# Kernel tuning notes

Hardware: AMD Instinct MI355X
Metric: run time of the kernel (lower is better)

## Reference

```python
import jax, jax.numpy as jnp
import numpy as np

N = 4096      # 2 ** var_num, var_num = 12
L = 50        # trajectory length
A_NUM = 4     # number of action variables (len(id2actvar))


def setup_inputs() -> dict:
    key = jax.random.key(0)
    ks = jax.random.split(key, 6)
    scale = 0.5 / np.sqrt(N)  # keep recurrence spectrally stable over L steps
    return {
        "init_states": jax.random.normal(ks[0], (N,), dtype=jnp.float32),
        "trajectories": jax.random.uniform(ks[1], (L, A_NUM), dtype=jnp.float32),
        "T_base": jax.random.normal(ks[2], (N, N), dtype=jnp.float32) * scale,
        "A_mats": jax.random.normal(ks[3], (A_NUM, N, N), dtype=jnp.float32) * (scale / A_NUM),
        "b": jax.random.normal(ks[4], (N,), dtype=jnp.float32) * 0.1,
        "r": jax.random.normal(ks[5], (N,), dtype=jnp.float32),
    }


def reference(init_states, trajectories, T_base, A_mats, b, r):
    # init_states is read from x in the original model but never used in the loop.
    n = T_base.shape[0]
    interface0 = jnp.zeros((n,), dtype=T_base.dtype)  # tf.zeros(2**var_num)

    def step(old_interface, act):
        # action-conditioned circuit filter: T_t = T_base + sum_a act[a] * A_mats[a]
        T = T_base + jnp.einsum('a,anm->nm', act, A_mats)
        new_interface = T @ old_interface + b          # [N]
        exp_reward = jnp.sum(r * new_interface)        # tf.reduce_sum(exp_reward)
        return new_interface, exp_reward

    _, exp_rewards = jax.lax.scan(step, interface0, trajectories)
    return exp_rewards  # [L]
```

## Files before the change

### kernel.cpp

```cpp
#include <hip/hip_runtime.h>
#include <hip/hip_fp16.h>

#define NDIM  4096
#define LSTEPS 50
#define ANUM   4
#define NMATS  5

__global__ void init_kernel(const float* __restrict__ b, const float* __restrict__ r,
                            float* __restrict__ x1, float* __restrict__ out) {
    const int tid = threadIdx.x;
    if (tid < LSTEPS) out[tid] = 0.0f;
    float part = 0.0f;
    for (int i = tid; i < NDIM; i += 256) {
        float bi = b[i];
        x1[i] = bi;
        part += r[i] * bi;
    }
#pragma unroll
    for (int off = 32; off > 0; off >>= 1) part += __shfl_xor(part, off, 64);
    __shared__ float sm[4];
    const int wave = tid >> 6, lane = tid & 63;
    if (lane == 0) sm[wave] = part;
    __syncthreads();
    if (tid == 0) out[0] = sm[0] + sm[1] + sm[2] + sm[3];
}

__global__ void conv_kernel(const float* __restrict__ Tb, const float* __restrict__ Am,
                            uint4* __restrict__ dst) {
    const size_t idx  = (size_t)blockIdx.x * 256 + threadIdx.x;
    const size_t base = idx * 8;
    const size_t nn   = (size_t)NDIM * NDIM;
    const float4* src;
    size_t off4;
    if (base < nn) { src = (const float4*)Tb; off4 = base >> 2; }
    else           { src = (const float4*)Am; off4 = (base - nn) >> 2; }
    const float4 f0 = src[off4];
    const float4 f1 = src[off4 + 1];
    union { uint4 v; __half h[8]; } pk;
    pk.h[0] = __float2half(f0.x); pk.h[1] = __float2half(f0.y);
    pk.h[2] = __float2half(f0.z); pk.h[3] = __float2half(f0.w);
    pk.h[4] = __float2half(f1.x); pk.h[5] = __float2half(f1.y);
    pk.h[6] = __float2half(f1.z); pk.h[7] = __float2half(f1.w);
    dst[idx] = pk.v;
}

__global__ __launch_bounds__(256) void step_half(
        const uint4* __restrict__ mats,
        const float* __restrict__ x_in,
        float*       __restrict__ x_out,
        const float* __restrict__ b,
        const float* __restrict__ r,
        const float* __restrict__ traj,
        float*       __restrict__ out, int t) {
    __shared__ float xs[NDIM];
    __shared__ float parts[4];
    const int tid = threadIdx.x;
    {
        const float4* xv  = (const float4*)x_in;
        float4*       xsv = (float4*)xs;
#pragma unroll
        for (int i = 0; i < 4; i++) xsv[tid + 256 * i] = xv[tid + 256 * i];
    }
    __syncthreads();

    const float a0 = traj[t * ANUM + 0], a1 = traj[t * ANUM + 1],
                a2 = traj[t * ANUM + 2], a3 = traj[t * ANUM + 3];

    const int wave = tid >> 6, lane = tid & 63;
    const int row  = blockIdx.x * 4 + wave;
    const size_t matq = (size_t)NDIM * NDIM / 8;
    const size_t rowq = (size_t)row * (NDIM / 8);

    float acc[NMATS] = {0.f, 0.f, 0.f, 0.f, 0.f};
#pragma unroll
    for (int c = 0; c < 8; c++) {
        const float4* xp = (const float4*)(&xs[c * 512 + lane * 8]);
        const float4 xa = xp[0], xb = xp[1];
        const size_t qi = rowq + (size_t)c * 64 + lane;
#pragma unroll
        for (int m = 0; m < NMATS; m++) {
            union { uint4 v; __half2 h2[4]; } u;
            u.v = mats[(size_t)m * matq + qi];
            const float2 p0 = __half22float2(u.h2[0]);
            const float2 p1 = __half22float2(u.h2[1]);
            const float2 p2 = __half22float2(u.h2[2]);
            const float2 p3 = __half22float2(u.h2[3]);
            float a = acc[m];
            a = fmaf(p0.x, xa.x, a); a = fmaf(p0.y, xa.y, a);
            a = fmaf(p1.x, xa.z, a); a = fmaf(p1.y, xa.w, a);
            a = fmaf(p2.x, xb.x, a); a = fmaf(p2.y, xb.y, a);
            a = fmaf(p3.x, xb.z, a); a = fmaf(p3.y, xb.w, a);
            acc[m] = a;
        }
    }
    float s = acc[0] + a0 * acc[1] + a1 * acc[2] + a2 * acc[3] + a3 * acc[4];
#pragma unroll
    for (int off = 32; off > 0; off >>= 1) s += __shfl_xor(s, off, 64);
    if (lane == 0) {
        const float y = s + b[row];
        x_out[row] = y;
        parts[wave] = r[row] * y;
    }
    __syncthreads();
    if (tid == 0) atomicAdd(out + t, parts[0] + parts[1] + parts[2] + parts[3]);
}

__global__ __launch_bounds__(256) void step_f32(
        const float* __restrict__ Tb, const float* __restrict__ Am,
        const float* __restrict__ x_in, float* __restrict__ x_out,
        const float* __restrict__ b, const float* __restrict__ r,
        const float* __restrict__ traj, float* __restrict__ out, int t) {
    __shared__ float xs[NDIM];
    __shared__ float parts[4];
    const int tid = threadIdx.x;
    {
        const float4* xv  = (const float4*)x_in;
        float4*       xsv = (float4*)xs;
#pragma unroll
        for (int i = 0; i < 4; i++) xsv[tid + 256 * i] = xv[tid + 256 * i];
    }
    __syncthreads();

    const float a0 = traj[t * ANUM + 0], a1 = traj[t * ANUM + 1],
                a2 = traj[t * ANUM + 2], a3 = traj[t * ANUM + 3];

    const int wave = tid >> 6, lane = tid & 63;
    const int row  = blockIdx.x * 4 + wave;
    const size_t nn = (size_t)NDIM * NDIM;
    const float4* mat[NMATS] = {
        (const float4*)Tb, (const float4*)Am, (const float4*)(Am + nn),
        (const float4*)(Am + 2 * nn), (const float4*)(Am + 3 * nn)};
    const size_t rowq = (size_t)row * (NDIM / 4);

    float acc[NMATS] = {0.f, 0.f, 0.f, 0.f, 0.f};
#pragma unroll
    for (int c = 0; c < 16; c++) {
        const float4 xa = *(const float4*)(&xs[c * 256 + lane * 4]);
        const size_t qi = rowq + (size_t)c * 64 + lane;
#pragma unroll
        for (int m = 0; m < NMATS; m++) {
            const float4 v = mat[m][qi];
            float a = acc[m];
            a = fmaf(v.x, xa.x, a); a = fmaf(v.y, xa.y, a);
            a = fmaf(v.z, xa.z, a); a = fmaf(v.w, xa.w, a);
            acc[m] = a;
        }
    }
    float s = acc[0] + a0 * acc[1] + a1 * acc[2] + a2 * acc[3] + a3 * acc[4];
#pragma unroll
    for (int off = 32; off > 0; off >>= 1) s += __shfl_xor(s, off, 64);
    if (lane == 0) {
        const float y = s + b[row];
        x_out[row] = y;
        parts[wave] = r[row] * y;
    }
    __syncthreads();
    if (tid == 0) atomicAdd(out + t, parts[0] + parts[1] + parts[2] + parts[3]);
}

extern "C" void kernel_launch(void* const* d_in, const int* in_sizes, int n_in,
                              void* d_out, int out_size, void* d_ws, size_t ws_size,
                              hipStream_t stream) {
    const float* traj = (const float*)d_in[1];
    const float* Tb   = (const float*)d_in[2];
    const float* Am   = (const float*)d_in[3];
    const float* b    = (const float*)d_in[4];
    const float* r    = (const float*)d_in[5];
    float* out = (float*)d_out;

    const size_t matBytes = (size_t)NMATS * NDIM * NDIM * sizeof(__half);
    const size_t xBytes   = 2 * (size_t)NDIM * sizeof(float);
    const bool useHalf = ws_size >= matBytes + xBytes;

    if (useHalf) {
        uint4* mats = (uint4*)d_ws;
        float* x0 = (float*)((char*)d_ws + matBytes);
        float* x1 = x0 + NDIM;
        init_kernel<<<1, 256, 0, stream>>>(b, r, x0, out);
        const int convBlocks = (int)(((size_t)NMATS * NDIM * NDIM / 8) / 256);
        conv_kernel<<<convBlocks, 256, 0, stream>>>(Tb, Am, mats);
        for (int t = 1; t < LSTEPS; t++) {
            float* xi = (t & 1) ? x0 : x1;
            float* xo = (t & 1) ? x1 : x0;
            step_half<<<NDIM / 4, 256, 0, stream>>>(mats, xi, xo, b, r, traj, out, t);
        }
    } else {
        float* x0 = (float*)d_ws;
        float* x1 = x0 + NDIM;
        init_kernel<<<1, 256, 0, stream>>>(b, r, x0, out);
        for (int t = 1; t < LSTEPS; t++) {
            float* xi = (t & 1) ? x0 : x1;
            float* xo = (t & 1) ? x1 : x0;
            step_f32<<<NDIM / 4, 256, 0, stream>>>(Tb, Am, xi, xo, b, r, traj, out, t);
        }
    }
}
```

Before: 1.987 ms.

## Precombine per-step fp16 matrices in chunks so each step reads one matrix

Instead of converting five matrices to fp16 once and streaming all five every step, a combine kernel folds T_base plus the action-weighted A_mats into one fp16 matrix per timestep, in two chunks of 25 and 24 steps. Each step then streams one 32MB matrix instead of five. The per-step reward is no longer accumulated with atomics; an extra block computes the dot product of the previous state, which drops the zero-init dependency. The cost is a large combine write (about 800MB per chunk) and a much larger workspace requirement, and nontemporal loads are used for the matrix stream.

```diff
diff --git a/kernel.cpp b/kernel.cpp
--- a/kernel.cpp
+++ b/kernel.cpp
@@ -1,145 +1,180 @@
 #include <hip/hip_runtime.h>
 #include <hip/hip_fp16.h>
 
-#define NDIM  4096
+#define NDIM   4096
 #define LSTEPS 50
 #define ANUM   4
-#define NMATS  5
-
-__global__ void init_kernel(const float* __restrict__ b, const float* __restrict__ r,
-                            float* __restrict__ x1, float* __restrict__ out) {
+#define NN     ((size_t)NDIM * (size_t)NDIM)
+#define CHUNK1 25
+#define CHUNK2 24
+
+typedef unsigned int nuint4 __attribute__((ext_vector_type(4)));
+typedef float        nfloat4 __attribute__((ext_vector_type(4)));
+
+__global__ void init_kernel(const float* __restrict__ b, float* __restrict__ x1) {
     const int tid = threadIdx.x;
-    if (tid < LSTEPS) out[tid] = 0.0f;
-    float part = 0.0f;
-    for (int i = tid; i < NDIM; i += 256) {
-        float bi = b[i];
-        x1[i] = bi;
-        part += r[i] * bi;
-    }
-#pragma unroll
-    for (int off = 32; off > 0; off >>= 1) part += __shfl_xor(part, off, 64);
-    __shared__ float sm[4];
-    const int wave = tid >> 6, lane = tid & 63;
-    if (lane == 0) sm[wave] = part;
+    const float4* bv = (const float4*)b;
+    float4* xv = (float4*)x1;
+#pragma unroll
+    for (int i = 0; i < 4; i++) xv[tid + 256 * i] = bv[tid + 256 * i];
+}
+
+__global__ __launch_bounds__(256) void combine_kernel(
+        const float* __restrict__ Tb, const float* __restrict__ Am,
+        const float* __restrict__ traj, uint4* __restrict__ outbuf,
+        int t0, int C) {
+    __shared__ float sact[CHUNK1 * ANUM];
+    const int tid = threadIdx.x;
+    if (tid < C * ANUM)
+        sact[tid] = traj[(size_t)(t0 + tid / ANUM) * ANUM + (tid % ANUM)];
     __syncthreads();
-    if (tid == 0) out[0] = sm[0] + sm[1] + sm[2] + sm[3];
-}
-
-__global__ void conv_kernel(const float* __restrict__ Tb, const float* __restrict__ Am,
-                            uint4* __restrict__ dst) {
-    const size_t idx  = (size_t)blockIdx.x * 256 + threadIdx.x;
-    const size_t base = idx * 8;
-    const size_t nn   = (size_t)NDIM * NDIM;
-    const float4* src;
-    size_t off4;
-    if (base < nn) { src = (const float4*)Tb; off4 = base >> 2; }
-    else           { src = (const float4*)Am; off4 = (base - nn) >> 2; }
-    const float4 f0 = src[off4];
-    const float4 f1 = src[off4 + 1];
-    union { uint4 v; __half h[8]; } pk;
-    pk.h[0] = __float2half(f0.x); pk.h[1] = __float2half(f0.y);
-    pk.h[2] = __float2half(f0.z); pk.h[3] = __float2half(f0.w);
-    pk.h[4] = __float2half(f1.x); pk.h[5] = __float2half(f1.y);
-    pk.h[6] = __float2half(f1.z); pk.h[7] = __float2half(f1.w);
-    dst[idx] = pk.v;
-}
-
-__global__ __launch_bounds__(256) void step_half(
-        const uint4* __restrict__ mats,
+
+    const size_t gtid = (size_t)blockIdx.x * 256 + tid;
+    const size_t e4   = gtid * 2;
+    const float4* tb4 = (const float4*)Tb;
+    const float4* am4 = (const float4*)Am;
+    const size_t m4 = NN / 4;
+
+    union F8 { float4 f4[2]; float f[8]; };
+    F8 tb, am[4];
+    tb.f4[0] = tb4[e4]; tb.f4[1] = tb4[e4 + 1];
+#pragma unroll
+    for (int m = 0; m < 4; m++) {
+        am[m].f4[0] = am4[(size_t)m * m4 + e4];
+        am[m].f4[1] = am4[(size_t)m * m4 + e4 + 1];
+    }
+
+    const size_t matq = NN / 8;
+    for (int t = 0; t < C; t++) {
+        const float w0 = sact[t * 4 + 0], w1 = sact[t * 4 + 1],
+                    w2 = sact[t * 4 + 2], w3 = sact[t * 4 + 3];
+        union { uint4 v; __half h[8]; } pk;
+#pragma unroll
+        for (int j = 0; j < 8; j++) {
+            float v = tb.f[j];
+            v = fmaf(w0, am[0].f[j], v);
+            v = fmaf(w1, am[1].f[j], v);
+            v = fmaf(w2, am[2].f[j], v);
+            v = fmaf(w3, am[3].f[j], v);
+            pk.h[j] = __float2half(v);
+        }
+        outbuf[(size_t)t * matq + gtid] = pk.v;
+    }
+}
+
+__global__ __launch_bounds__(256) void step_kernel(
+        const uint4* __restrict__ Tt,
         const float* __restrict__ x_in,
         float*       __restrict__ x_out,
         const float* __restrict__ b,
         const float* __restrict__ r,
-        const float* __restrict__ traj,
         float*       __restrict__ out, int t) {
-    __shared__ float xs[NDIM];
+    const int tid  = threadIdx.x;
+    const int wave = tid >> 6, lane = tid & 63;
+
+    if (blockIdx.x == gridDim.x - 1) {
+        __shared__ float parts[4];
+        float s = 0.f;
+#pragma unroll
+        for (int i = 0; i < 16; i++) {
+            const int idx = tid + 256 * i;
+            s = fmaf(r[idx], x_in[idx], s);
+        }
+#pragma unroll
+        for (int off = 32; off > 0; off >>= 1) s += __shfl_xor(s, off, 64);
+        if (lane == 0) parts[wave] = s;
+        __syncthreads();
+        if (tid == 0) out[t - 1] = parts[0] + parts[1] + parts[2] + parts[3];
+        return;
+    }
+
+    const int row = blockIdx.x * 4 + wave;
+    const size_t rowq = (size_t)row * (NDIM / 8);
+    const nuint4* Tn = (const nuint4*)Tt;
+    const float4* xv = (const float4*)x_in;
+
+    float acc = 0.f;
+#pragma unroll
+    for (int c = 0; c < 8; c++) {
+        const int ci = c * 64 + lane;
+        const nuint4 tv = __builtin_nontemporal_load(&Tn[rowq + ci]);
+        const float4 xa = xv[ci * 2];
+        const float4 xb = xv[ci * 2 + 1];
+        union { nuint4 v; __half2 h2[4]; } u; u.v = tv;
+        const float2 p0 = __half22float2(u.h2[0]);
+        const float2 p1 = __half22float2(u.h2[1]);
+        const float2 p2 = __half22float2(u.h2[2]);
+        const float2 p3 = __half22float2(u.h2[3]);
+        acc = fmaf(p0.x, xa.x, acc); acc = fmaf(p0.y, xa.y, acc);
+        acc = fmaf(p1.x, xa.z, acc); acc = fmaf(p1.y, xa.w, acc);
+        acc = fmaf(p2.x, xb.x, acc); acc = fmaf(p2.y, xb.y, acc);
+        acc = fmaf(p3.x, xb.z, acc); acc = fmaf(p3.y, xb.w, acc);
+    }
+#pragma unroll
+    for (int off = 32; off > 0; off >>= 1) acc += __shfl_xor(acc, off, 64);
+    if (lane == 0) x_out[row] = acc + b[row];
+}
+
+__global__ void dot_kernel(const float* __restrict__ x, const float* __restrict__ r,
+                           float* __restrict__ out_elem) {
+    const int tid = threadIdx.x;
+    const int wave = tid >> 6, lane = tid & 63;
     __shared__ float parts[4];
-    const int tid = threadIdx.x;
-    {
-        const float4* xv  = (const float4*)x_in;
-        float4*       xsv = (float4*)xs;
-#pragma unroll
-        for (int i = 0; i < 4; i++) xsv[tid + 256 * i] = xv[tid + 256 * i];
-    }
+    float s = 0.f;
+#pragma unroll
+    for (int i = 0; i < 16; i++) {
+        const int idx = tid + 256 * i;
+        s = fmaf(r[idx], x[idx], s);
+    }
+#pragma unroll
+    for (int off = 32; off > 0; off >>= 1) s += __shfl_xor(s, off, 64);
+    if (lane == 0) parts[wave] = s;
     __syncthreads();
-
-    const float a0 = traj[t * ANUM + 0], a1 = traj[t * ANUM + 1],
-                a2 = traj[t * ANUM + 2], a3 = traj[t * ANUM + 3];
-
-    const int wave = tid >> 6, lane = tid & 63;
-    const int row  = blockIdx.x * 4 + wave;
-    const size_t matq = (size_t)NDIM * NDIM / 8;
-    const size_t rowq = (size_t)row * (NDIM / 8);
-
-    float acc[NMATS] = {0.f, 0.f, 0.f, 0.f, 0.f};
-#pragma unroll
-    for (int c = 0; c < 8; c++) {
-        const float4* xp = (const float4*)(&xs[c * 512 + lane * 8]);
-        const float4 xa = xp[0], xb = xp[1];
-        const size_t qi = rowq + (size_t)c * 64 + lane;
-#pragma unroll
-        for (int m = 0; m < NMATS; m++) {
-            union { uint4 v; __half2 h2[4]; } u;
-            u.v = mats[(size_t)m * matq + qi];
-            const float2 p0 = __half22float2(u.h2[0]);
-            const float2 p1 = __half22float2(u.h2[1]);
-            const float2 p2 = __half22float2(u.h2[2]);
-            const float2 p3 = __half22float2(u.h2[3]);
-            float a = acc[m];
-            a = fmaf(p0.x, xa.x, a); a = fmaf(p0.y, xa.y, a);
-            a = fmaf(p1.x, xa.z, a); a = fmaf(p1.y, xa.w, a);
-            a = fmaf(p2.x, xb.x, a); a = fmaf(p2.y, xb.y, a);
-            a = fmaf(p3.x, xb.z, a); a = fmaf(p3.y, xb.w, a);
-            acc[m] = a;
-        }
-    }
-    float s = acc[0] + a0 * acc[1] + a1 * acc[2] + a2 * acc[3] + a3 * acc[4];
-#pragma unroll
-    for (int off = 32; off > 0; off >>= 1) s += __shfl_xor(s, off, 64);
-    if (lane == 0) {
-        const float y = s + b[row];
-        x_out[row] = y;
-        parts[wave] = r[row] * y;
-    }
-    __syncthreads();
-    if (tid == 0) atomicAdd(out + t, parts[0] + parts[1] + parts[2] + parts[3]);
-}
-
-__global__ __launch_bounds__(256) void step_f32(
+    if (tid == 0) *out_elem = parts[0] + parts[1] + parts[2] + parts[3];
+}
+
+__global__ __launch_bounds__(256) void step_f32_kernel(
         const float* __restrict__ Tb, const float* __restrict__ Am,
         const float* __restrict__ x_in, float* __restrict__ x_out,
         const float* __restrict__ b, const float* __restrict__ r,
         const float* __restrict__ traj, float* __restrict__ out, int t) {
-    __shared__ float xs[NDIM];
-    __shared__ float parts[4];
-    const int tid = threadIdx.x;
-    {
-        const float4* xv  = (const float4*)x_in;
-        float4*       xsv = (float4*)xs;
-#pragma unroll
-        for (int i = 0; i < 4; i++) xsv[tid + 256 * i] = xv[tid + 256 * i];
-    }
-    __syncthreads();
+    const int tid  = threadIdx.x;
+    const int wave = tid >> 6, lane = tid & 63;
+
+    if (blockIdx.x == gridDim.x - 1) {
+        __shared__ float parts[4];
+        float s = 0.f;
+#pragma unroll
+        for (int i = 0; i < 16; i++) {
+            const int idx = tid + 256 * i;
+            s = fmaf(r[idx], x_in[idx], s);
+        }
+#pragma unroll
+        for (int off = 32; off > 0; off >>= 1) s += __shfl_xor(s, off, 64);
+        if (lane == 0) parts[wave] = s;
+        __syncthreads();
+        if (tid == 0) out[t - 1] = parts[0] + parts[1] + parts[2] + parts[3];
+        return;
+    }
 
     const float a0 = traj[t * ANUM + 0], a1 = traj[t * ANUM + 1],
                 a2 = traj[t * ANUM + 2], a3 = traj[t * ANUM + 3];
-
-    const int wave = tid >> 6, lane = tid & 63;
-    const int row  = blockIdx.x * 4 + wave;
-    const size_t nn = (size_t)NDIM * NDIM;
-    const float4* mat[NMATS] = {
-        (const float4*)Tb, (const float4*)Am, (const float4*)(Am + nn),
-        (const float4*)(Am + 2 * nn), (const float4*)(Am + 3 * nn)};
+    const int row = blockIdx.x * 4 + wave;
+    const nfloat4* mat[5] = {
+        (const nfloat4*)Tb, (const nfloat4*)Am, (const nfloat4*)(Am + NN),
+        (const nfloat4*)(Am + 2 * NN), (const nfloat4*)(Am + 3 * NN)};
     const size_t rowq = (size_t)row * (NDIM / 4);
-
-    float acc[NMATS] = {0.f, 0.f, 0.f, 0.f, 0.f};
+    const float4* xv = (const float4*)x_in;
+
+    float acc[5] = {0.f, 0.f, 0.f, 0.f, 0.f};
 #pragma unroll
     for (int c = 0; c < 16; c++) {
-        const float4 xa = *(const float4*)(&xs[c * 256 + lane * 4]);
-        const size_t qi = rowq + (size_t)c * 64 + lane;
-#pragma unroll
-        for (int m = 0; m < NMATS; m++) {
-            const float4 v = mat[m][qi];
+        const int ci = c * 64 + lane;
+        const float4 xa = xv[ci];
+        const size_t qi = rowq + ci;
+#pragma unroll
+        for (int m = 0; m < 5; m++) {
+            const nfloat4 v = __builtin_nontemporal_load(&mat[m][qi]);
             float a = acc[m];
             a = fmaf(v.x, xa.x, a); a = fmaf(v.y, xa.y, a);
             a = fmaf(v.z, xa.z, a); a = fmaf(v.w, xa.w, a);
@@ -149,13 +184,7 @@
     float s = acc[0] + a0 * acc[1] + a1 * acc[2] + a2 * acc[3] + a3 * acc[4];
 #pragma unroll
     for (int off = 32; off > 0; off >>= 1) s += __shfl_xor(s, off, 64);
-    if (lane == 0) {
-        const float y = s + b[row];
-        x_out[row] = y;
-        parts[wave] = r[row] * y;
-    }
-    __syncthreads();
-    if (tid == 0) atomicAdd(out + t, parts[0] + parts[1] + parts[2] + parts[3]);
+    if (lane == 0) x_out[row] = s + b[row];
 }
 
 extern "C" void kernel_launch(void* const* d_in, const int* in_sizes, int n_in,
@@ -168,30 +197,45 @@
     const float* r    = (const float*)d_in[5];
     float* out = (float*)d_out;
 
-    const size_t matBytes = (size_t)NMATS * NDIM * NDIM * sizeof(__half);
-    const size_t xBytes   = 2 * (size_t)NDIM * sizeof(float);
-    const bool useHalf = ws_size >= matBytes + xBytes;
-
-    if (useHalf) {
-        uint4* mats = (uint4*)d_ws;
-        float* x0 = (float*)((char*)d_ws + matBytes);
+    const size_t chunkBytes = (size_t)CHUNK1 * NN * sizeof(__half);
+    const size_t xBytes     = 2 * (size_t)NDIM * sizeof(float);
+    const bool useChunks = ws_size >= chunkBytes + xBytes;
+
+    if (useChunks) {
+        uint4* chunk = (uint4*)d_ws;
+        float* x0 = (float*)((char*)d_ws + chunkBytes);
         float* x1 = x0 + NDIM;
-        init_kernel<<<1, 256, 0, stream>>>(b, r, x0, out);
-        const int convBlocks = (int)(((size_t)NMATS * NDIM * NDIM / 8) / 256);
-        conv_kernel<<<convBlocks, 256, 0, stream>>>(Tb, Am, mats);
+        const size_t matq = NN / 8;
+        const int combBlocks = (int)(matq / 256);
+
+        init_kernel<<<1, 256, 0, stream>>>(b, x0);
+
+        combine_kernel<<<combBlocks, 256, 0, stream>>>(Tb, Am, traj, chunk, 1, CHUNK1);
+        for (int t = 1; t <= CHUNK1; t++) {
+            float* xi = (t & 1) ? x0 : x1;
+            float* xo = (t & 1) ? x1 : x0;
+            step_kernel<<<NDIM / 4 + 1, 256, 0, stream>>>(
+                chunk + (size_t)(t - 1) * matq, xi, xo, b, r, out, t);
+        }
+        combine_kernel<<<combBlocks, 256, 0, stream>>>(Tb, Am, traj, chunk,
+                                                       CHUNK1 + 1, CHUNK2);
+        for (int t = CHUNK1 + 1; t < LSTEPS; t++) {
+            float* xi = (t & 1) ? x0 : x1;
+            float* xo = (t & 1) ? x1 : x0;
+            step_kernel<<<NDIM / 4 + 1, 256, 0, stream>>>(
+                chunk + (size_t)(t - CHUNK1 - 1) * matq, xi, xo, b, r, out, t);
+        }
+        dot_kernel<<<1, 256, 0, stream>>>(x1, r, out + (LSTEPS - 1));
+    } else {
+        float* x0 = (float*)d_ws;
+        float* x1 = x0 + NDIM;
+        init_kernel<<<1, 256, 0, stream>>>(b, x0);
         for (int t = 1; t < LSTEPS; t++) {
             float* xi = (t & 1) ? x0 : x1;
             float* xo = (t & 1) ? x1 : x0;
-            step_half<<<NDIM / 4, 256, 0, stream>>>(mats, xi, xo, b, r, traj, out, t);
-        }
-    } else {
-        float* x0 = (float*)d_ws;
-        float* x1 = x0 + NDIM;
-        init_kernel<<<1, 256, 0, stream>>>(b, r, x0, out);
-        for (int t = 1; t < LSTEPS; t++) {
-            float* xi = (t & 1) ? x0 : x1;
-            float* xo = (t & 1) ? x1 : x0;
-            step_f32<<<NDIM / 4, 256, 0, stream>>>(Tb, Am, xi, xo, b, r, traj, out, t);
-        }
-    }
-}
+            step_f32_kernel<<<NDIM / 4 + 1, 256, 0, stream>>>(Tb, Am, xi, xo, b, r,
+                                                              traj, out, t);
+        }
+        dot_kernel<<<1, 256, 0, stream>>>(x1, r, out + (LSTEPS - 1));
+    }
+}
```

Result: faster. 1.709 ms (-14.0%).
